# Optimization experiments

Hardware: AMD Instinct MI355X
Metric: run time of the kernel (lower is better)

The kernel has to match this reference:

```python
import jax, jax.numpy as jnp
import numpy as np

N = 50000
E = 800000
IN_DIM = 128
HID = 64
HEADS = 4
OUT_DIM = 64
NEG_SLOPE = 0.2


def setup_inputs() -> dict:
    key = jax.random.key(0)
    ks = jax.random.split(key, 10)
    x = jax.random.normal(ks[0], (N, IN_DIM), dtype=jnp.float32)
    edge_index = jax.random.randint(ks[1], (2, E), 0, N, dtype=jnp.int64)
    s1 = 1.0 / np.sqrt(IN_DIM)
    s2 = 1.0 / np.sqrt(HEADS * HID)
    return {
        "x": x,
        "edge_index": edge_index,
        "W1": jax.random.normal(ks[2], (IN_DIM, HEADS * HID), dtype=jnp.float32) * s1,
        "a_src1": jax.random.normal(ks[3], (HEADS, HID), dtype=jnp.float32) * s2,
        "a_dst1": jax.random.normal(ks[4], (HEADS, HID), dtype=jnp.float32) * s2,
        "b1": jnp.zeros((HEADS * HID,), dtype=jnp.float32),
        "W2": jax.random.normal(ks[5], (HEADS * HID, OUT_DIM), dtype=jnp.float32) * s2,
        "a_src2": jax.random.normal(ks[6], (1, OUT_DIM), dtype=jnp.float32) * 0.125,
        "a_dst2": jax.random.normal(ks[7], (1, OUT_DIM), dtype=jnp.float32) * 0.125,
        "b2": jnp.zeros((OUT_DIM,), dtype=jnp.float32),
    }


def gat_layer(x, src, dst, W, a_src, a_dst, bias, heads, ch, concat):
    n = x.shape[0]
    h = (x @ W).reshape(n, heads, ch)                      # [N,H,C]
    asrc = jnp.einsum('nhc,hc->nh', h, a_src)              # [N,H]
    adst = jnp.einsum('nhc,hc->nh', h, a_dst)              # [N,H]
    e = asrc[src] + adst[dst]                              # [E',H]
    e = jnp.where(e > 0, e, NEG_SLOPE * e)                 # LeakyReLU(0.2)
    # segment softmax over incoming edges of each dst node
    m = jax.ops.segment_max(e, dst, num_segments=n)        # [N,H]
    m = jnp.where(jnp.isfinite(m), m, 0.0)
    ex = jnp.exp(e - m[dst])
    denom = jax.ops.segment_sum(ex, dst, num_segments=n)   # [N,H]
    alpha = ex / (denom[dst] + 1e-16)                      # [E',H]
    out = jax.ops.segment_sum(alpha[:, :, None] * h[src], dst, num_segments=n)  # [N,H,C]
    if concat:
        out = out.reshape(n, heads * ch)
    else:
        out = out.mean(axis=1)
    return out + bias


def reference(x, edge_index, W1, a_src1, a_dst1, b1, W2, a_src2, a_dst2, b2):
    n = x.shape[0]
    loops = jnp.arange(n, dtype=edge_index.dtype)
    src = jnp.concatenate([edge_index[0], loops])          # add self-loops (PyG default)
    dst = jnp.concatenate([edge_index[1], loops])
    h = gat_layer(x, src, dst, W1, a_src1, a_dst1, b1, HEADS, HID, True)
    h = jax.nn.elu(h)
    out = gat_layer(h, src, dst, W2, a_src2, a_dst2, b2, 1, OUT_DIM, False)
    return out
```

## Files before the change

kernel.cpp:

```cpp
#include <hip/hip_runtime.h>
#include <hip/hip_bf16.h>

#define NN 50000
#define EE 800000
#define IN_DIM 128
#define HH 256
#define HID 64
#define HEADS 4
#define OUT_DIM 64
#define SCAN_BLOCKS 196

static __device__ __forceinline__ unsigned short f2bf(float f) {
    unsigned int u = __float_as_uint(f);
    u += 0x7fffu + ((u >> 16) & 1u);
    return (unsigned short)(u >> 16);
}
static __device__ __forceinline__ float bf2f(unsigned short h) {
    return __uint_as_float(((unsigned int)h) << 16);
}


__global__ void hist_kernel(const int* __restrict__ ei, int* __restrict__ deg) {
    int e = blockIdx.x * 256 + threadIdx.x;
    atomicAdd(&deg[ei[EE + e]], 1);
}

__global__ __launch_bounds__(256) void block_scan_kernel(
    const int* __restrict__ deg, int* __restrict__ local_scan,
    int* __restrict__ block_sum) {
    __shared__ int tmp[256];
    int t = threadIdx.x, i = blockIdx.x * 256 + t;
    int v = (i < NN) ? deg[i] : 0;
    tmp[t] = v;
    __syncthreads();
    for (int d = 1; d < 256; d <<= 1) {
        int u = (t >= d) ? tmp[t - d] : 0;
        __syncthreads();
        tmp[t] += u;
        __syncthreads();
    }
    if (i < NN) local_scan[i] = tmp[t] - v;
    if (t == 255) block_sum[blockIdx.x] = tmp[255];
}

__global__ __launch_bounds__(256) void scan_sums_kernel(int* __restrict__ block_sum) {
    __shared__ int tmp[256];
    int t = threadIdx.x;
    int v = (t < SCAN_BLOCKS) ? block_sum[t] : 0;
    tmp[t] = v;
    __syncthreads();
    for (int d = 1; d < 256; d <<= 1) {
        int u = (t >= d) ? tmp[t - d] : 0;
        __syncthreads();
        tmp[t] += u;
        __syncthreads();
    }
    if (t < SCAN_BLOCKS) block_sum[t] = tmp[t] - v;
}

__global__ __launch_bounds__(256) void finalize_kernel(
    const int* __restrict__ local_scan, const int* __restrict__ block_sum,
    int* __restrict__ row_ptr, int* __restrict__ cursor) {
    int i = blockIdx.x * 256 + threadIdx.x;
    if (i < NN) {
        int v = local_scan[i] + block_sum[blockIdx.x];
        row_ptr[i] = v; cursor[i] = v;
    }
    if (i == 0) row_ptr[NN] = EE;
}

__global__ void scatter_kernel(const int* __restrict__ ei, int* __restrict__ cursor,
                               int* __restrict__ edge_src) {
    int e = blockIdx.x * 256 + threadIdx.x;
    int d = ei[EE + e];
    int pos = atomicAdd(&cursor[d], 1);
    edge_src[pos] = ei[e];
}


__global__ __launch_bounds__(256) void gemm1_kernel(
    const float* __restrict__ x, const float* __restrict__ W1,
    const float* __restrict__ a_src1, const float* __restrict__ a_dst1,
    unsigned short* __restrict__ h1, float* __restrict__ asrc1, float* __restrict__ adst1) {
    __shared__ __align__(16) float xs[64][IN_DIM];
    int t = threadIdx.x;
    int row0 = blockIdx.x * 64;
    #pragma unroll
    for (int j = 0; j < 8; j++) {
        int idx = t + j * 256;
        int r = idx >> 5, k4 = (idx & 31) * 4;
        int rr = row0 + r; if (rr >= NN) rr = NN - 1;
        *reinterpret_cast<float4*>(&xs[r][k4]) =
            *reinterpret_cast<const float4*>(&x[(size_t)rr * IN_DIM + k4]);
    }
    __syncthreads();
    int lane = t & 63, wid = t >> 6;
    float4 acc[16];
    #pragma unroll
    for (int r = 0; r < 16; r++) acc[r] = make_float4(0.f, 0.f, 0.f, 0.f);
    const float* wbase = W1 + lane * 4;
    for (int k = 0; k < IN_DIM; k += 4) {
        float4 w0 = *reinterpret_cast<const float4*>(&wbase[(k + 0) * HH]);
        float4 w1 = *reinterpret_cast<const float4*>(&wbase[(k + 1) * HH]);
        float4 w2 = *reinterpret_cast<const float4*>(&wbase[(k + 2) * HH]);
        float4 w3 = *reinterpret_cast<const float4*>(&wbase[(k + 3) * HH]);
        #pragma unroll
        for (int r = 0; r < 16; r++) {
            float4 xv = *reinterpret_cast<const float4*>(&xs[wid * 16 + r][k]);
            acc[r].x = fmaf(xv.x, w0.x, acc[r].x); acc[r].y = fmaf(xv.x, w0.y, acc[r].y);
            acc[r].z = fmaf(xv.x, w0.z, acc[r].z); acc[r].w = fmaf(xv.x, w0.w, acc[r].w);
            acc[r].x = fmaf(xv.y, w1.x, acc[r].x); acc[r].y = fmaf(xv.y, w1.y, acc[r].y);
            acc[r].z = fmaf(xv.y, w1.z, acc[r].z); acc[r].w = fmaf(xv.y, w1.w, acc[r].w);
            acc[r].x = fmaf(xv.z, w2.x, acc[r].x); acc[r].y = fmaf(xv.z, w2.y, acc[r].y);
            acc[r].z = fmaf(xv.z, w2.z, acc[r].z); acc[r].w = fmaf(xv.z, w2.w, acc[r].w);
            acc[r].x = fmaf(xv.w, w3.x, acc[r].x); acc[r].y = fmaf(xv.w, w3.y, acc[r].y);
            acc[r].z = fmaf(xv.w, w3.z, acc[r].z); acc[r].w = fmaf(xv.w, w3.w, acc[r].w);
        }
    }
    float4 asv = *reinterpret_cast<const float4*>(&a_src1[lane * 4]);
    float4 adv = *reinterpret_cast<const float4*>(&a_dst1[lane * 4]);
    int head = lane >> 4;
    #pragma unroll
    for (int r = 0; r < 16; r++) {
        int row = row0 + wid * 16 + r;
        bool ok = row < NN;
        if (ok) {
            ushort4 hv;
            hv.x = f2bf(acc[r].x); hv.y = f2bf(acc[r].y);
            hv.z = f2bf(acc[r].z); hv.w = f2bf(acc[r].w);
            *reinterpret_cast<ushort4*>(&h1[(size_t)row * HH + lane * 4]) = hv;
        }
        float vs = acc[r].x * asv.x + acc[r].y * asv.y + acc[r].z * asv.z + acc[r].w * asv.w;
        float vd = acc[r].x * adv.x + acc[r].y * adv.y + acc[r].z * adv.z + acc[r].w * adv.w;
        #pragma unroll
        for (int o = 1; o < 16; o <<= 1) { vs += __shfl_xor(vs, o); vd += __shfl_xor(vd, o); }
        if (ok && (lane & 15) == 0) {
            asrc1[row * HEADS + head] = vs;
            adst1[row * HEADS + head] = vd;
        }
    }
}


__global__ __launch_bounds__(256) void agg1_kernel(
    const int* __restrict__ row_ptr, const int* __restrict__ edge_src,
    const unsigned short* __restrict__ h1, const float* __restrict__ asrc1,
    const float* __restrict__ adst1, const float* __restrict__ b1,
    float* __restrict__ x2) {
    int wid = threadIdx.x >> 6, lane = threadIdx.x & 63;
    int node = blockIdx.x * 4 + wid;
    int head = lane >> 4;
    float ad = adst1[node * HEADS + head];
    int beg = row_ptr[node], end = row_ptr[node + 1];
    float denom = 0.f;
    float ax = 0.f, ay = 0.f, az = 0.f, aw = 0.f;
    int sA = (beg < end) ? edge_src[beg] : node;
    int sB = (beg + 1 < end) ? edge_src[beg + 1] : node;
    float eA = asrc1[sA * HEADS + head];
    float eB = asrc1[sB * HEADS + head];
    ushort4 hA = *reinterpret_cast<const ushort4*>(&h1[(size_t)sA * HH + lane * 4]);
    ushort4 hB = *reinterpret_cast<const ushort4*>(&h1[(size_t)sB * HH + lane * 4]);
    for (int i = beg; i <= end; i++) {
        int j = i + 2;
        int sC = (j < end) ? edge_src[j] : node;
        float eC = asrc1[sC * HEADS + head];
        ushort4 hC = *reinterpret_cast<const ushort4*>(&h1[(size_t)sC * HH + lane * 4]);
        float e = eA + ad;
        e = e > 0.f ? e : 0.2f * e;
        float ex = __expf(e);
        denom += ex;
        ax = fmaf(ex, bf2f(hA.x), ax); ay = fmaf(ex, bf2f(hA.y), ay);
        az = fmaf(ex, bf2f(hA.z), az); aw = fmaf(ex, bf2f(hA.w), aw);
        eA = eB; hA = hB;
        eB = eC; hB = hC;
    }
    float inv = 1.0f / (denom + 1e-16f);
    int cb = lane * 4;
    float v0 = ax * inv + b1[cb + 0];
    float v1 = ay * inv + b1[cb + 1];
    float v2 = az * inv + b1[cb + 2];
    float v3 = aw * inv + b1[cb + 3];
    v0 = v0 > 0.f ? v0 : (__expf(v0) - 1.f);
    v1 = v1 > 0.f ? v1 : (__expf(v1) - 1.f);
    v2 = v2 > 0.f ? v2 : (__expf(v2) - 1.f);
    v3 = v3 > 0.f ? v3 : (__expf(v3) - 1.f);
    float4 o; o.x = v0; o.y = v1; o.z = v2; o.w = v3;
    *reinterpret_cast<float4*>(&x2[(size_t)node * HH + cb]) = o;
}


__global__ __launch_bounds__(256) void gemm2_kernel(
    const float* __restrict__ x2, const float* __restrict__ W2,
    const float* __restrict__ a_src2, const float* __restrict__ a_dst2,
    unsigned short* __restrict__ h2, float* __restrict__ asrc2, float* __restrict__ adst2) {
    __shared__ __align__(16) float xs[16][HH];
    int t = threadIdx.x;
    int row0 = blockIdx.x * 16;
    #pragma unroll
    for (int j = 0; j < 4; j++) {
        int idx = t + j * 256;
        int r = idx >> 6, k4 = (idx & 63) * 4;
        *reinterpret_cast<float4*>(&xs[r][k4]) =
            *reinterpret_cast<const float4*>(&x2[(size_t)(row0 + r) * HH + k4]);
    }
    __syncthreads();
    int c = t & 63, rg = t >> 6;
    float acc[4] = {0.f, 0.f, 0.f, 0.f};
    for (int k = 0; k < HH; k += 4) {
        float w0 = W2[(k + 0) * OUT_DIM + c];
        float w1 = W2[(k + 1) * OUT_DIM + c];
        float w2 = W2[(k + 2) * OUT_DIM + c];
        float w3 = W2[(k + 3) * OUT_DIM + c];
        #pragma unroll
        for (int i = 0; i < 4; i++) {
            int r = rg + i * 4;
            float4 xv = *reinterpret_cast<const float4*>(&xs[r][k]);
            acc[i] = fmaf(xv.x, w0, acc[i]);
            acc[i] = fmaf(xv.y, w1, acc[i]);
            acc[i] = fmaf(xv.z, w2, acc[i]);
            acc[i] = fmaf(xv.w, w3, acc[i]);
        }
    }
    float as = a_src2[c], ad = a_dst2[c];
    #pragma unroll
    for (int i = 0; i < 4; i++) {
        int row = row0 + rg + i * 4;
        h2[(size_t)row * OUT_DIM + c] = f2bf(acc[i]);
        float vs = acc[i] * as, vd = acc[i] * ad;
        #pragma unroll
        for (int o = 32; o > 0; o >>= 1) { vs += __shfl_xor(vs, o); vd += __shfl_xor(vd, o); }
        if (c == 0) { asrc2[row] = vs; adst2[row] = vd; }
    }
}


__global__ __launch_bounds__(256) void agg2_kernel(
    const int* __restrict__ row_ptr, const int* __restrict__ edge_src,
    const unsigned short* __restrict__ h2, const float* __restrict__ asrc2,
    const float* __restrict__ adst2, const float* __restrict__ b2,
    float* __restrict__ out) {
    int wid = threadIdx.x >> 6, lane = threadIdx.x & 63;
    int node = blockIdx.x * 4 + wid;
    float ad = adst2[node];
    int beg = row_ptr[node], end = row_ptr[node + 1];
    float denom = 0.f, acc = 0.f;
    int sA = (beg < end) ? edge_src[beg] : node;
    int sB = (beg + 1 < end) ? edge_src[beg + 1] : node;
    float eA = asrc2[sA], eB = asrc2[sB];
    unsigned short hA = h2[(size_t)sA * OUT_DIM + lane];
    unsigned short hB = h2[(size_t)sB * OUT_DIM + lane];
    for (int i = beg; i <= end; i++) {
        int j = i + 2;
        int sC = (j < end) ? edge_src[j] : node;
        float eC = asrc2[sC];
        unsigned short hC = h2[(size_t)sC * OUT_DIM + lane];
        float e = eA + ad;
        e = e > 0.f ? e : 0.2f * e;
        float ex = __expf(e);
        denom += ex;
        acc = fmaf(ex, bf2f(hA), acc);
        eA = eB; hA = hB;
        eB = eC; hB = hC;
    }
    out[(size_t)node * OUT_DIM + lane] = acc / (denom + 1e-16f) + b2[lane];
}


extern "C" void kernel_launch(void* const* d_in, const int* in_sizes, int n_in,
                              void* d_out, int out_size, void* d_ws, size_t ws_size,
                              hipStream_t stream) {
    const float* x   = (const float*)d_in[0];
    const int*   ei  = (const int*)d_in[1];
    const float* W1  = (const float*)d_in[2];
    const float* as1 = (const float*)d_in[3];
    const float* ad1 = (const float*)d_in[4];
    const float* b1  = (const float*)d_in[5];
    const float* W2  = (const float*)d_in[6];
    const float* as2 = (const float*)d_in[7];
    const float* ad2 = (const float*)d_in[8];
    const float* b2  = (const float*)d_in[9];
    float* out = (float*)d_out;

    char* ws = (char*)d_ws;
    size_t off = 0;
    auto alloc = [&](size_t bytes) -> void* {
        void* p = ws + off;
        off += (bytes + 255) & ~(size_t)255;
        return p;
    };
    unsigned short* h1 = (unsigned short*)alloc((size_t)NN * HH * 2);
    float* x2     = (float*)alloc((size_t)NN * HH * 4);
    unsigned short* h2 = (unsigned short*)alloc((size_t)NN * OUT_DIM * 2);
    float* asrc1  = (float*)alloc((size_t)NN * HEADS * 4);
    float* adst1  = (float*)alloc((size_t)NN * HEADS * 4);
    float* asrc2  = (float*)alloc((size_t)NN * 4);
    float* adst2  = (float*)alloc((size_t)NN * 4);
    int*   deg    = (int*)alloc((size_t)NN * 4);
    int*   row_ptr= (int*)alloc((size_t)(NN + 1) * 4);
    int*   cursor = (int*)alloc((size_t)NN * 4);
    int*   edge_src=(int*)alloc((size_t)EE * 4);
    int*   local_scan = (int*)alloc((size_t)NN * 4);
    int*   block_sum  = (int*)alloc((size_t)SCAN_BLOCKS * 4);

    hipMemsetAsync(deg, 0, (size_t)NN * 4, stream);
    hist_kernel<<<EE / 256, 256, 0, stream>>>(ei, deg);
    block_scan_kernel<<<SCAN_BLOCKS, 256, 0, stream>>>(deg, local_scan, block_sum);
    scan_sums_kernel<<<1, 256, 0, stream>>>(block_sum);
    finalize_kernel<<<SCAN_BLOCKS, 256, 0, stream>>>(local_scan, block_sum, row_ptr, cursor);
    scatter_kernel<<<EE / 256, 256, 0, stream>>>(ei, cursor, edge_src);

    gemm1_kernel<<<(NN + 63) / 64, 256, 0, stream>>>(x, W1, as1, ad1, h1, asrc1, adst1);
    agg1_kernel<<<NN / 4, 256, 0, stream>>>(row_ptr, edge_src, h1, asrc1, adst1, b1, x2);
    gemm2_kernel<<<NN / 16, 256, 0, stream>>>(x2, W2, as2, ad2, h2, asrc2, adst2);
    agg2_kernel<<<NN / 4, 256, 0, stream>>>(row_ptr, edge_src, h2, asrc2, adst2, b2, out);
}
```

Measured before the change: 398.7 us.

## Fuse gemm1 with degree histogram, grid-stride aggregation, deeper prefetch, retile gemm2

Merges the degree histogram into the first GEMM launch by giving extra blocks the histogram work, and shrinks the GEMM1 tile to 32 rows so it launches more blocks. The aggregation kernels become grid-stride loops over a fixed set of warps, with a three-deep gather prefetch instead of two. GEMM2 now uses 32-row tiles with 8 rows per wave and bounds checks. This trims launch count and aims to add memory-level parallelism in the gathers, at the cost of less register reuse in GEMM1 and possible load imbalance in the strided node loops.

New measurement: 398.3 us. About the same (-0.1%).

```diff
diff --git a/kernel.cpp b/kernel.cpp
--- a/kernel.cpp
+++ b/kernel.cpp
@@ -9,6 +9,10 @@
 #define HEADS 4
 #define OUT_DIM 64
 #define SCAN_BLOCKS 196
+#define G1_BLOCKS 1563
+#define HIST_BLOCKS 3125
+#define AGG_BLOCKS 1563
+#define TOTW (AGG_BLOCKS * 4)
 
 static __device__ __forceinline__ unsigned short f2bf(float f) {
     unsigned int u = __float_as_uint(f);
@@ -20,10 +24,75 @@
 }
 
 
-__global__ void hist_kernel(const int* __restrict__ ei, int* __restrict__ deg) {
-    int e = blockIdx.x * 256 + threadIdx.x;
-    atomicAdd(&deg[ei[EE + e]], 1);
-}
+__global__ __launch_bounds__(256) void gemm1_hist_kernel(
+    const float* __restrict__ x, const float* __restrict__ W1,
+    const float* __restrict__ a_src1, const float* __restrict__ a_dst1,
+    unsigned short* __restrict__ h1, float* __restrict__ asrc1, float* __restrict__ adst1,
+    const int* __restrict__ ei, int* __restrict__ deg) {
+    if (blockIdx.x >= G1_BLOCKS) {
+        int e = (blockIdx.x - G1_BLOCKS) * 256 + threadIdx.x;
+        atomicAdd(&deg[ei[EE + e]], 1);
+        return;
+    }
+    __shared__ __align__(16) float xs[32][IN_DIM];
+    int t = threadIdx.x;
+    int row0 = blockIdx.x * 32;
+    #pragma unroll
+    for (int j = 0; j < 4; j++) {
+        int idx = t + j * 256;
+        int r = idx >> 5, k4 = (idx & 31) * 4;
+        int rr = row0 + r; if (rr >= NN) rr = NN - 1;
+        *reinterpret_cast<float4*>(&xs[r][k4]) =
+            *reinterpret_cast<const float4*>(&x[(size_t)rr * IN_DIM + k4]);
+    }
+    __syncthreads();
+    int lane = t & 63, wid = t >> 6;
+    float4 acc[8];
+    #pragma unroll
+    for (int r = 0; r < 8; r++) acc[r] = make_float4(0.f, 0.f, 0.f, 0.f);
+    const float* wbase = W1 + lane * 4;
+    for (int k = 0; k < IN_DIM; k += 4) {
+        float4 w0 = *reinterpret_cast<const float4*>(&wbase[(k + 0) * HH]);
+        float4 w1 = *reinterpret_cast<const float4*>(&wbase[(k + 1) * HH]);
+        float4 w2 = *reinterpret_cast<const float4*>(&wbase[(k + 2) * HH]);
+        float4 w3 = *reinterpret_cast<const float4*>(&wbase[(k + 3) * HH]);
+        #pragma unroll
+        for (int r = 0; r < 8; r++) {
+            float4 xv = *reinterpret_cast<const float4*>(&xs[wid * 8 + r][k]);
+            acc[r].x = fmaf(xv.x, w0.x, acc[r].x); acc[r].y = fmaf(xv.x, w0.y, acc[r].y);
+            acc[r].z = fmaf(xv.x, w0.z, acc[r].z); acc[r].w = fmaf(xv.x, w0.w, acc[r].w);
+            acc[r].x = fmaf(xv.y, w1.x, acc[r].x); acc[r].y = fmaf(xv.y, w1.y, acc[r].y);
+            acc[r].z = fmaf(xv.y, w1.z, acc[r].z); acc[r].w = fmaf(xv.y, w1.w, acc[r].w);
+            acc[r].x = fmaf(xv.z, w2.x, acc[r].x); acc[r].y = fmaf(xv.z, w2.y, acc[r].y);
+            acc[r].z = fmaf(xv.z, w2.z, acc[r].z); acc[r].w = fmaf(xv.z, w2.w, acc[r].w);
+            acc[r].x = fmaf(xv.w, w3.x, acc[r].x); acc[r].y = fmaf(xv.w, w3.y, acc[r].y);
+            acc[r].z = fmaf(xv.w, w3.z, acc[r].z); acc[r].w = fmaf(xv.w, w3.w, acc[r].w);
+        }
+    }
+    float4 asv = *reinterpret_cast<const float4*>(&a_src1[lane * 4]);
+    float4 adv = *reinterpret_cast<const float4*>(&a_dst1[lane * 4]);
+    int head = lane >> 4;
+    #pragma unroll
+    for (int r = 0; r < 8; r++) {
+        int row = row0 + wid * 8 + r;
+        bool ok = row < NN;
+        if (ok) {
+            ushort4 hv;
+            hv.x = f2bf(acc[r].x); hv.y = f2bf(acc[r].y);
+            hv.z = f2bf(acc[r].z); hv.w = f2bf(acc[r].w);
+            *reinterpret_cast<ushort4*>(&h1[(size_t)row * HH + lane * 4]) = hv;
+        }
+        float vs = acc[r].x * asv.x + acc[r].y * asv.y + acc[r].z * asv.z + acc[r].w * asv.w;
+        float vd = acc[r].x * adv.x + acc[r].y * adv.y + acc[r].z * adv.z + acc[r].w * adv.w;
+        #pragma unroll
+        for (int o = 1; o < 16; o <<= 1) { vs += __shfl_xor(vs, o); vd += __shfl_xor(vd, o); }
+        if (ok && (lane & 15) == 0) {
+            asrc1[row * HEADS + head] = vs;
+            adst1[row * HEADS + head] = vd;
+        }
+    }
+}
+
 
 __global__ __launch_bounds__(256) void block_scan_kernel(
     const int* __restrict__ deg, int* __restrict__ local_scan,
@@ -78,114 +147,59 @@
 }
 
 
-__global__ __launch_bounds__(256) void gemm1_kernel(
-    const float* __restrict__ x, const float* __restrict__ W1,
-    const float* __restrict__ a_src1, const float* __restrict__ a_dst1,
-    unsigned short* __restrict__ h1, float* __restrict__ asrc1, float* __restrict__ adst1) {
-    __shared__ __align__(16) float xs[64][IN_DIM];
-    int t = threadIdx.x;
-    int row0 = blockIdx.x * 64;
-    #pragma unroll
-    for (int j = 0; j < 8; j++) {
-        int idx = t + j * 256;
-        int r = idx >> 5, k4 = (idx & 31) * 4;
-        int rr = row0 + r; if (rr >= NN) rr = NN - 1;
-        *reinterpret_cast<float4*>(&xs[r][k4]) =
-            *reinterpret_cast<const float4*>(&x[(size_t)rr * IN_DIM + k4]);
-    }
-    __syncthreads();
-    int lane = t & 63, wid = t >> 6;
-    float4 acc[16];
-    #pragma unroll
-    for (int r = 0; r < 16; r++) acc[r] = make_float4(0.f, 0.f, 0.f, 0.f);
-    const float* wbase = W1 + lane * 4;
-    for (int k = 0; k < IN_DIM; k += 4) {
-        float4 w0 = *reinterpret_cast<const float4*>(&wbase[(k + 0) * HH]);
-        float4 w1 = *reinterpret_cast<const float4*>(&wbase[(k + 1) * HH]);
-        float4 w2 = *reinterpret_cast<const float4*>(&wbase[(k + 2) * HH]);
-        float4 w3 = *reinterpret_cast<const float4*>(&wbase[(k + 3) * HH]);
-        #pragma unroll
-        for (int r = 0; r < 16; r++) {
-            float4 xv = *reinterpret_cast<const float4*>(&xs[wid * 16 + r][k]);
-            acc[r].x = fmaf(xv.x, w0.x, acc[r].x); acc[r].y = fmaf(xv.x, w0.y, acc[r].y);
-            acc[r].z = fmaf(xv.x, w0.z, acc[r].z); acc[r].w = fmaf(xv.x, w0.w, acc[r].w);
-            acc[r].x = fmaf(xv.y, w1.x, acc[r].x); acc[r].y = fmaf(xv.y, w1.y, acc[r].y);
-            acc[r].z = fmaf(xv.y, w1.z, acc[r].z); acc[r].w = fmaf(xv.y, w1.w, acc[r].w);
-            acc[r].x = fmaf(xv.z, w2.x, acc[r].x); acc[r].y = fmaf(xv.z, w2.y, acc[r].y);
-            acc[r].z = fmaf(xv.z, w2.z, acc[r].z); acc[r].w = fmaf(xv.z, w2.w, acc[r].w);
-            acc[r].x = fmaf(xv.w, w3.x, acc[r].x); acc[r].y = fmaf(xv.w, w3.y, acc[r].y);
-            acc[r].z = fmaf(xv.w, w3.z, acc[r].z); acc[r].w = fmaf(xv.w, w3.w, acc[r].w);
-        }
-    }
-    float4 asv = *reinterpret_cast<const float4*>(&a_src1[lane * 4]);
-    float4 adv = *reinterpret_cast<const float4*>(&a_dst1[lane * 4]);
-    int head = lane >> 4;
-    #pragma unroll
-    for (int r = 0; r < 16; r++) {
-        int row = row0 + wid * 16 + r;
-        bool ok = row < NN;
-        if (ok) {
-            ushort4 hv;
-            hv.x = f2bf(acc[r].x); hv.y = f2bf(acc[r].y);
-            hv.z = f2bf(acc[r].z); hv.w = f2bf(acc[r].w);
-            *reinterpret_cast<ushort4*>(&h1[(size_t)row * HH + lane * 4]) = hv;
-        }
-        float vs = acc[r].x * asv.x + acc[r].y * asv.y + acc[r].z * asv.z + acc[r].w * asv.w;
-        float vd = acc[r].x * adv.x + acc[r].y * adv.y + acc[r].z * adv.z + acc[r].w * adv.w;
-        #pragma unroll
-        for (int o = 1; o < 16; o <<= 1) { vs += __shfl_xor(vs, o); vd += __shfl_xor(vd, o); }
-        if (ok && (lane & 15) == 0) {
-            asrc1[row * HEADS + head] = vs;
-            adst1[row * HEADS + head] = vd;
-        }
-    }
-}
-
-
 __global__ __launch_bounds__(256) void agg1_kernel(
     const int* __restrict__ row_ptr, const int* __restrict__ edge_src,
     const unsigned short* __restrict__ h1, const float* __restrict__ asrc1,
     const float* __restrict__ adst1, const float* __restrict__ b1,
     float* __restrict__ x2) {
     int wid = threadIdx.x >> 6, lane = threadIdx.x & 63;
-    int node = blockIdx.x * 4 + wid;
+    int gw = blockIdx.x * 4 + wid;
     int head = lane >> 4;
-    float ad = adst1[node * HEADS + head];
-    int beg = row_ptr[node], end = row_ptr[node + 1];
-    float denom = 0.f;
-    float ax = 0.f, ay = 0.f, az = 0.f, aw = 0.f;
-    int sA = (beg < end) ? edge_src[beg] : node;
-    int sB = (beg + 1 < end) ? edge_src[beg + 1] : node;
-    float eA = asrc1[sA * HEADS + head];
-    float eB = asrc1[sB * HEADS + head];
-    ushort4 hA = *reinterpret_cast<const ushort4*>(&h1[(size_t)sA * HH + lane * 4]);
-    ushort4 hB = *reinterpret_cast<const ushort4*>(&h1[(size_t)sB * HH + lane * 4]);
-    for (int i = beg; i <= end; i++) {
-        int j = i + 2;
-        int sC = (j < end) ? edge_src[j] : node;
-        float eC = asrc1[sC * HEADS + head];
-        ushort4 hC = *reinterpret_cast<const ushort4*>(&h1[(size_t)sC * HH + lane * 4]);
-        float e = eA + ad;
-        e = e > 0.f ? e : 0.2f * e;
-        float ex = __expf(e);
-        denom += ex;
-        ax = fmaf(ex, bf2f(hA.x), ax); ay = fmaf(ex, bf2f(hA.y), ay);
-        az = fmaf(ex, bf2f(hA.z), az); aw = fmaf(ex, bf2f(hA.w), aw);
-        eA = eB; hA = hB;
-        eB = eC; hB = hC;
-    }
-    float inv = 1.0f / (denom + 1e-16f);
-    int cb = lane * 4;
-    float v0 = ax * inv + b1[cb + 0];
-    float v1 = ay * inv + b1[cb + 1];
-    float v2 = az * inv + b1[cb + 2];
-    float v3 = aw * inv + b1[cb + 3];
-    v0 = v0 > 0.f ? v0 : (__expf(v0) - 1.f);
-    v1 = v1 > 0.f ? v1 : (__expf(v1) - 1.f);
-    v2 = v2 > 0.f ? v2 : (__expf(v2) - 1.f);
-    v3 = v3 > 0.f ? v3 : (__expf(v3) - 1.f);
-    float4 o; o.x = v0; o.y = v1; o.z = v2; o.w = v3;
-    *reinterpret_cast<float4*>(&x2[(size_t)node * HH + cb]) = o;
+    unsigned cb = lane * 4;
+    const unsigned short* h1l = h1 + cb;
+    const float* asl = asrc1 + head;
+    float4 bv = *reinterpret_cast<const float4*>(&b1[cb]);
+    for (int node = gw; node < NN; node += TOTW) {
+        float ad = adst1[node * HEADS + head];
+        int beg = row_ptr[node], end = row_ptr[node + 1];
+        float denom = 0.f;
+        float ax = 0.f, ay = 0.f, az = 0.f, aw = 0.f;
+        int s0 = (beg < end) ? edge_src[beg] : node;
+        int s1 = (beg + 1 < end) ? edge_src[beg + 1] : node;
+        int s2 = (beg + 2 < end) ? edge_src[beg + 2] : node;
+        float e0 = asl[(unsigned)s0 * HEADS];
+        float e1 = asl[(unsigned)s1 * HEADS];
+        float e2 = asl[(unsigned)s2 * HEADS];
+        ushort4 h0 = *reinterpret_cast<const ushort4*>(&h1l[(unsigned)s0 * HH]);
+        ushort4 h1v = *reinterpret_cast<const ushort4*>(&h1l[(unsigned)s1 * HH]);
+        ushort4 h2v = *reinterpret_cast<const ushort4*>(&h1l[(unsigned)s2 * HH]);
+        for (int i = beg; i <= end; i++) {
+            int j = i + 3;
+            int s3 = (j < end) ? edge_src[j] : node;
+            float e3 = asl[(unsigned)s3 * HEADS];
+            ushort4 h3 = *reinterpret_cast<const ushort4*>(&h1l[(unsigned)s3 * HH]);
+            float e = e0 + ad;
+            e = fmaxf(e, 0.2f * e);
+            float ex = __expf(e);
+            denom += ex;
+            ax = fmaf(ex, bf2f(h0.x), ax); ay = fmaf(ex, bf2f(h0.y), ay);
+            az = fmaf(ex, bf2f(h0.z), az); aw = fmaf(ex, bf2f(h0.w), aw);
+            e0 = e1; h0 = h1v;
+            e1 = e2; h1v = h2v;
+            e2 = e3; h2v = h3;
+        }
+        float inv = 1.0f / (denom + 1e-16f);
+        float v0 = ax * inv + bv.x;
+        float v1 = ay * inv + bv.y;
+        float v2 = az * inv + bv.z;
+        float v3 = aw * inv + bv.w;
+        v0 = v0 > 0.f ? v0 : (__expf(v0) - 1.f);
+        v1 = v1 > 0.f ? v1 : (__expf(v1) - 1.f);
+        v2 = v2 > 0.f ? v2 : (__expf(v2) - 1.f);
+        v3 = v3 > 0.f ? v3 : (__expf(v3) - 1.f);
+        float4 o; o.x = v0; o.y = v1; o.z = v2; o.w = v3;
+        *reinterpret_cast<float4*>(&x2[(size_t)node * HH + cb]) = o;
+    }
 }
 
 
@@ -193,43 +207,46 @@
     const float* __restrict__ x2, const float* __restrict__ W2,
     const float* __restrict__ a_src2, const float* __restrict__ a_dst2,
     unsigned short* __restrict__ h2, float* __restrict__ asrc2, float* __restrict__ adst2) {
-    __shared__ __align__(16) float xs[16][HH];
+    __shared__ __align__(16) float xs[32][HH];
     int t = threadIdx.x;
-    int row0 = blockIdx.x * 16;
-    #pragma unroll
-    for (int j = 0; j < 4; j++) {
+    int row0 = blockIdx.x * 32;
+    #pragma unroll
+    for (int j = 0; j < 8; j++) {
         int idx = t + j * 256;
         int r = idx >> 6, k4 = (idx & 63) * 4;
+        int rr = row0 + r; if (rr >= NN) rr = NN - 1;
         *reinterpret_cast<float4*>(&xs[r][k4]) =
-            *reinterpret_cast<const float4*>(&x2[(size_t)(row0 + r) * HH + k4]);
+            *reinterpret_cast<const float4*>(&x2[(size_t)rr * HH + k4]);
     }
     __syncthreads();
-    int c = t & 63, rg = t >> 6;
-    float acc[4] = {0.f, 0.f, 0.f, 0.f};
+    int c = t & 63, wid = t >> 6;
+    float acc[8];
+    #pragma unroll
+    for (int r = 0; r < 8; r++) acc[r] = 0.f;
     for (int k = 0; k < HH; k += 4) {
         float w0 = W2[(k + 0) * OUT_DIM + c];
         float w1 = W2[(k + 1) * OUT_DIM + c];
         float w2 = W2[(k + 2) * OUT_DIM + c];
         float w3 = W2[(k + 3) * OUT_DIM + c];
         #pragma unroll
-        for (int i = 0; i < 4; i++) {
-            int r = rg + i * 4;
-            float4 xv = *reinterpret_cast<const float4*>(&xs[r][k]);
-            acc[i] = fmaf(xv.x, w0, acc[i]);
-            acc[i] = fmaf(xv.y, w1, acc[i]);
-            acc[i] = fmaf(xv.z, w2, acc[i]);
-            acc[i] = fmaf(xv.w, w3, acc[i]);
+        for (int r = 0; r < 8; r++) {
+            float4 xv = *reinterpret_cast<const float4*>(&xs[wid * 8 + r][k]);
+            acc[r] = fmaf(xv.x, w0, acc[r]);
+            acc[r] = fmaf(xv.y, w1, acc[r]);
+            acc[r] = fmaf(xv.z, w2, acc[r]);
+            acc[r] = fmaf(xv.w, w3, acc[r]);
         }
     }
     float as = a_src2[c], ad = a_dst2[c];
     #pragma unroll
-    for (int i = 0; i < 4; i++) {
-        int row = row0 + rg + i * 4;
-        h2[(size_t)row * OUT_DIM + c] = f2bf(acc[i]);
-        float vs = acc[i] * as, vd = acc[i] * ad;
+    for (int r = 0; r < 8; r++) {
+        int row = row0 + wid * 8 + r;
+        bool ok = row < NN;
+        if (ok) h2[(size_t)row * OUT_DIM + c] = f2bf(acc[r]);
+        float vs = acc[r] * as, vd = acc[r] * ad;
         #pragma unroll
         for (int o = 32; o > 0; o >>= 1) { vs += __shfl_xor(vs, o); vd += __shfl_xor(vd, o); }
-        if (c == 0) { asrc2[row] = vs; adst2[row] = vd; }
+        if (ok && c == 0) { asrc2[row] = vs; adst2[row] = vd; }
     }
 }
 
@@ -240,29 +257,36 @@
     const float* __restrict__ adst2, const float* __restrict__ b2,
     float* __restrict__ out) {
     int wid = threadIdx.x >> 6, lane = threadIdx.x & 63;
-    int node = blockIdx.x * 4 + wid;
-    float ad = adst2[node];
-    int beg = row_ptr[node], end = row_ptr[node + 1];
-    float denom = 0.f, acc = 0.f;
-    int sA = (beg < end) ? edge_src[beg] : node;
-    int sB = (beg + 1 < end) ? edge_src[beg + 1] : node;
-    float eA = asrc2[sA], eB = asrc2[sB];
-    unsigned short hA = h2[(size_t)sA * OUT_DIM + lane];
-    unsigned short hB = h2[(size_t)sB * OUT_DIM + lane];
-    for (int i = beg; i <= end; i++) {
-        int j = i + 2;
-        int sC = (j < end) ? edge_src[j] : node;
-        float eC = asrc2[sC];
-        unsigned short hC = h2[(size_t)sC * OUT_DIM + lane];
-        float e = eA + ad;
-        e = e > 0.f ? e : 0.2f * e;
-        float ex = __expf(e);
-        denom += ex;
-        acc = fmaf(ex, bf2f(hA), acc);
-        eA = eB; hA = hB;
-        eB = eC; hB = hC;
-    }
-    out[(size_t)node * OUT_DIM + lane] = acc / (denom + 1e-16f) + b2[lane];
+    int gw = blockIdx.x * 4 + wid;
+    const unsigned short* h2l = h2 + lane;
+    float bl = b2[lane];
+    for (int node = gw; node < NN; node += TOTW) {
+        float ad = adst2[node];
+        int beg = row_ptr[node], end = row_ptr[node + 1];
+        float denom = 0.f, acc = 0.f;
+        int s0 = (beg < end) ? edge_src[beg] : node;
+        int s1 = (beg + 1 < end) ? edge_src[beg + 1] : node;
+        int s2 = (beg + 2 < end) ? edge_src[beg + 2] : node;
+        float e0 = asrc2[s0], e1 = asrc2[s1], e2 = asrc2[s2];
+        unsigned short h0 = h2l[(unsigned)s0 * OUT_DIM];
+        unsigned short h1v = h2l[(unsigned)s1 * OUT_DIM];
+        unsigned short h2v = h2l[(unsigned)s2 * OUT_DIM];
+        for (int i = beg; i <= end; i++) {
+            int j = i + 3;
+            int s3 = (j < end) ? edge_src[j] : node;
+            float e3 = asrc2[s3];
+            unsigned short h3 = h2l[(unsigned)s3 * OUT_DIM];
+            float e = e0 + ad;
+            e = fmaxf(e, 0.2f * e);
+            float ex = __expf(e);
+            denom += ex;
+            acc = fmaf(ex, bf2f(h0), acc);
+            e0 = e1; h0 = h1v;
+            e1 = e2; h1v = h2v;
+            e2 = e3; h2v = h3;
+        }
+        out[(size_t)node * OUT_DIM + lane] = acc / (denom + 1e-16f) + bl;
+    }
 }
 
 
@@ -303,14 +327,14 @@
     int*   block_sum  = (int*)alloc((size_t)SCAN_BLOCKS * 4);
 
     hipMemsetAsync(deg, 0, (size_t)NN * 4, stream);
-    hist_kernel<<<EE / 256, 256, 0, stream>>>(ei, deg);
+    gemm1_hist_kernel<<<G1_BLOCKS + HIST_BLOCKS, 256, 0, stream>>>(
+        x, W1, as1, ad1, h1, asrc1, adst1, ei, deg);
     block_scan_kernel<<<SCAN_BLOCKS, 256, 0, stream>>>(deg, local_scan, block_sum);
     scan_sums_kernel<<<1, 256, 0, stream>>>(block_sum);
     finalize_kernel<<<SCAN_BLOCKS, 256, 0, stream>>>(local_scan, block_sum, row_ptr, cursor);
     scatter_kernel<<<EE / 256, 256, 0, stream>>>(ei, cursor, edge_src);
 
-    gemm1_kernel<<<(NN + 63) / 64, 256, 0, stream>>>(x, W1, as1, ad1, h1, asrc1, adst1);
-    agg1_kernel<<<NN / 4, 256, 0, stream>>>(row_ptr, edge_src, h1, asrc1, adst1, b1, x2);
-    gemm2_kernel<<<NN / 16, 256, 0, stream>>>(x2, W2, as2, ad2, h2, asrc2, adst2);
-    agg2_kernel<<<NN / 4, 256, 0, stream>>>(row_ptr, edge_src, h2, asrc2, adst2, b2, out);
-}
+    agg1_kernel<<<AGG_BLOCKS, 256, 0, stream>>>(row_ptr, edge_src, h1, asrc1, adst1, b1, x2);
+    gemm2_kernel<<<(NN + 31) / 32, 256, 0, stream>>>(x2, W2, as2, ad2, h2, asrc2, adst2);
+    agg2_kernel<<<AGG_BLOCKS, 256, 0, stream>>>(row_ptr, edge_src, h2, asrc2, adst2, b2, out);
+}
```
